# Optimization experiments

Hardware: AMD Instinct MI355X
Metric: run time of the kernel (lower is better)

## Reference

```python
import jax, jax.numpy as jnp
import numpy as np

MARGIN = 0.0
GAP = 0.4
N, D, C = 8192, 128, 10


def setup_inputs() -> dict:
    key = jax.random.key(0)
    k1, k2, k3 = jax.random.split(key, 3)
    inputs = jax.random.normal(k1, (N, D), dtype=jnp.float32)
    pred = jax.random.normal(k2, (N, C), dtype=jnp.float32)
    targets = jax.random.randint(k3, (N,), 0, C, dtype=jnp.int64)
    return {"inputs": inputs, "pred": pred, "targets": targets}


def reference(inputs, pred, targets):
    n = inputs.shape[0]
    # pairwise euclidean distances: ||xi||^2 + ||xj||^2 - 2 xi.xj, clamped + sqrt
    sq = jnp.sum(inputs * inputs, axis=1)                      # [n]
    dist = sq[:, None] + sq[None, :] - 2.0 * (inputs @ inputs.T)
    dist = jnp.sqrt(jnp.clip(dist, 1e-12))                     # [n, n]
    same = targets[:, None] == targets[None, :]                # [n, n] bool

    # confusion detection (original runs under no_grad)
    p = jax.nn.softmax(jax.lax.stop_gradient(pred), axis=1)
    val, top2 = jax.lax.top_k(p, 2)                            # [n,2]
    confuse = (val[:, 0] - val[:, 1] <= GAP) | (top2[:, 0] != targets)  # [n]

    # hard mining per row: hardest positive (max over same-class), hardest negative (min over diff-class)
    dist_ap = jnp.max(jnp.where(same, dist, -jnp.inf), axis=1)  # [n]
    dist_an = jnp.min(jnp.where(same, jnp.inf, dist), axis=1)   # [n]

    # MarginRankingLoss(margin=MARGIN) with y=1: mean(relu(-(an - ap) + margin)) over confused rows
    per_row = jnp.maximum(dist_ap - dist_an + MARGIN, 0.0)
    cnt = jnp.sum(confuse.astype(jnp.float32))
    loss = jnp.sum(jnp.where(confuse, per_row, 0.0)) / jnp.maximum(cnt, 1.0)
    return jnp.where(cnt > 0, loss, 0.0)
```

## Files before the change

kernel.cpp:

```cpp
#include <hip/hip_runtime.h>

#define NROWS 8192
#define DIMX  128
#define KB    192
#define KSEG  12
#define PTB   24576
#define NKS   3
#define NCLS  10
#define GAPV  0.4f
#define DEBIAS 504.03125f
#define SCL   (-0.0078125f)
#define RGR   256
#define NRG   (NROWS / RGR)
#define CHUNK 512
#define NCHUNK (NROWS / CHUNK)
#define SLAB  64
#define NSLAB (CHUNK / SLAB)

typedef __attribute__((ext_vector_type(4))) int i32x4;

#define GLOAD_LDS16(g, l)                                              \
  __builtin_amdgcn_global_load_lds(                                    \
      (const __attribute__((address_space(1))) void*)(g),              \
      (__attribute__((address_space(3))) void*)(l), 16, 0, 0)

__device__ __forceinline__ int q8(float v) {
  int q = (int)rintf(16.f * v);
  return q > 127 ? 127 : (q < -127 ? -127 : q);
}

__global__ __launch_bounds__(256) void prep_k(const float* __restrict__ x,
                                              const int* __restrict__ tgt,
                                              const float* __restrict__ pred,
                                              char* __restrict__ xa,
                                              char* __restrict__ xbm,
                                              float* __restrict__ sq,
                                              int* __restrict__ conf,
                                              unsigned* __restrict__ ctrs) {
  if (blockIdx.x == 0 && threadIdx.x < 3) ctrs[threadIdx.x] = 0u;

  const int wave = threadIdx.x >> 6;
  const int lane = threadIdx.x & 63;
  const int row  = blockIdx.x * 4 + wave;
  const float2 f2 = ((const float2*)(x + (size_t)row * DIMX))[lane];
  float s = f2.x * f2.x + f2.y * f2.y;
  #pragma unroll
  for (int m = 1; m < 64; m <<= 1) s += __shfl_xor(s, m, 64);

  char* basea = xa  + (size_t)(row >> 7) * PTB + (size_t)(row & 127) * 16;
  char* baseb = xbm + (size_t)(row >> 7) * PTB + (size_t)(row & 127) * 16;
  {
    const int q0 = q8(f2.x), q1 = q8(f2.y);
    const unsigned short u = (unsigned short)((q0 & 0xFF) | ((q1 & 0xFF) << 8));
    const size_t off = (size_t)(lane >> 3) * 2048 + (lane & 7) * 2;
    *(unsigned short*)(basea + off) = u;
    *(unsigned short*)(baseb + off) = u;
  }
  const int cls = tgt[row];
  if (lane < 32) {
    const int j = 2 * lane;
    const int c = j >> 2;
    const bool hit = (c < NCLS) && (c == cls);
    const unsigned short ua = hit ? (unsigned short)0x7F7F : 0;
    const unsigned short ub = hit ? (unsigned short)0x8181 : 0;
    const size_t off = (size_t)(8 + (j >> 4)) * 2048 + (j & 15);
    *(unsigned short*)(basea + off) = ua;
    *(unsigned short*)(baseb + off) = ub;
  }

  if (lane == 0) {
    sq[row] = s;
    const float* pp = pred + (size_t)row * NCLS;
    float v[NCLS];
    #pragma unroll
    for (int c = 0; c < NCLS; ++c) v[c] = pp[c];
    float m1 = v[0]; int i1 = 0;
    #pragma unroll
    for (int c = 1; c < NCLS; ++c)
      if (v[c] > m1) { m1 = v[c]; i1 = c; }
    float m2 = -INFINITY, sum = 0.f;
    #pragma unroll
    for (int c = 0; c < NCLS; ++c) {
      sum += __expf(v[c] - m1);
      if (c != i1) m2 = fmaxf(m2, v[c]);
    }
    const float d01 = (1.f - __expf(m2 - m1)) / sum;
    conf[row] = (d01 <= GAPV) || (i1 != cls);
  }
}

__global__ __launch_bounds__(256)
__attribute__((amdgpu_waves_per_eu(3, 4)))
void gram_k(const char* __restrict__ xa,
            const char* __restrict__ xbm,
            const float* __restrict__ sq,
            float* __restrict__ smax,
            float* __restrict__ smin) {
  __shared__ char  ldsb[2][KSEG * 1024];
  __shared__ float sqb[2][SLAB];
  const int tid  = threadIdx.x;
  const int wave = tid >> 6;
  const int lane = tid & 63;
  const int quad = lane >> 4;
  const int m16  = lane & 15;
  const int bx = blockIdx.x, by = blockIdx.y;

  i32x4 A[4][NKS];
  #pragma unroll
  for (int rt = 0; rt < 4; ++rt) {
    const int rbase = wave * 64 + rt * 16;
    const char* pa = xa + (size_t)(bx * 2 + (rbase >> 7)) * PTB
                        + (size_t)((rbase & 127) + m16) * 16;
    #pragma unroll
    for (int ks = 0; ks < NKS; ++ks)
      A[rt][ks] = *(const i32x4*)(pa + (size_t)(ks * 4 + quad) * 2048);
  }
  #pragma unroll
  for (int rt = 0; rt < 4; ++rt)
    #pragma unroll
    for (int ks = 0; ks < NKS; ++ks)
      asm("" : "+v"(A[rt][ks]));

  float gmin[4][4], gmax[4][4];
  #pragma unroll
  for (int r = 0; r < 4; ++r)
    #pragma unroll
    for (int q = 0; q < 4; ++q) { gmin[r][q] = INFINITY; gmax[r][q] = -INFINITY; }

  {
    const char* srcb = xbm + (size_t)(by * 4) * PTB;
    #pragma unroll
    for (int u = 0; u < 3; ++u) {
      const int kseg = wave * 3 + u;
      GLOAD_LDS16(srcb + (size_t)kseg * 2048 + lane * 16, &ldsb[0][kseg * 1024 + lane * 16]);
    }
    if (wave == 3 && lane < 16)
      GLOAD_LDS16((const char*)(sq + by * CHUNK) + lane * 16, (char*)&sqb[0][0] + lane * 16);
  }

  for (int s = 0; s < NSLAB; ++s) {
    __syncthreads();
    if (s + 1 < NSLAB) {
      const char* srcb = xbm + (size_t)(by * 4 + ((s + 1) >> 1)) * PTB + ((s + 1) & 1) * 1024;
      char* dstb = &ldsb[(s + 1) & 1][0];
      #pragma unroll
      for (int u = 0; u < 3; ++u) {
        const int kseg = wave * 3 + u;
        GLOAD_LDS16(srcb + (size_t)kseg * 2048 + lane * 16, dstb + kseg * 1024 + lane * 16);
      }
      if (wave == 3 && lane < 16)
        GLOAD_LDS16((const char*)(sq + by * CHUNK + (s + 1) * SLAB) + lane * 16,
                    (char*)&sqb[(s + 1) & 1][0] + lane * 16);
    }
    const char* buf = &ldsb[s & 1][0];
    #pragma unroll
    for (int jt = 0; jt < 4; ++jt) {
      i32x4 B[NKS];
      #pragma unroll
      for (int ks = 0; ks < NKS; ++ks)
        B[ks] = *(const i32x4*)(buf + (ks * 4 + quad) * 1024 + (jt * 16 + m16) * 16);
      const float sqj = sqb[s & 1][jt * 16 + m16];

      i32x4 acc[4];
      #pragma unroll
      for (int r = 0; r < 4; ++r) acc[r] = (i32x4){0, 0, 0, 0};
      #pragma unroll
      for (int ks = 0; ks < NKS; ++ks)
        #pragma unroll
        for (int r = 0; r < 4; ++r)
          acc[r] = __builtin_amdgcn_mfma_i32_16x16x64_i8(A[r][ks], B[ks], acc[r], 0, 0, 0);

      #pragma unroll
      for (int r = 0; r < 4; ++r)
        #pragma unroll
        for (int q = 0; q < 4; ++q) {
          const float cand = fmaf((float)acc[r][q], SCL, sqj);
          gmin[r][q] = fminf(gmin[r][q], cand);
          gmax[r][q] = fmaxf(gmax[r][q], cand);
        }
    }
  }

  #pragma unroll
  for (int m = 1; m <= 8; m <<= 1)
    #pragma unroll
    for (int r = 0; r < 4; ++r)
      #pragma unroll
      for (int q = 0; q < 4; ++q) {
        gmin[r][q] = fminf(gmin[r][q], __shfl_xor(gmin[r][q], m, 64));
        gmax[r][q] = fmaxf(gmax[r][q], __shfl_xor(gmax[r][q], m, 64));
      }

  if (m16 == 0) {
    const size_t sidx = (size_t)(bx * NCHUNK + by) * RGR;
    #pragma unroll
    for (int r = 0; r < 4; ++r) {
      const int lrow = wave * 64 + r * 16 + quad * 4;
      *(float4*)&smax[sidx + lrow] = make_float4(gmax[r][0], gmax[r][1], gmax[r][2], gmax[r][3]);
      *(float4*)&smin[sidx + lrow] = make_float4(gmin[r][0], gmin[r][1], gmin[r][2], gmin[r][3]);
    }
  }
}

__global__ __launch_bounds__(256) void reduce_k(const float* __restrict__ smax,
                                                const float* __restrict__ smin,
                                                const float* __restrict__ sq,
                                                const int* __restrict__ conf,
                                                unsigned* __restrict__ ctrs,
                                                float* __restrict__ out) {
  __shared__ float red[2][4];
  const int tid = threadIdx.x, bx = blockIdx.x;
  const int wave = tid >> 6, lane = tid & 63;
  const int row = bx * RGR + tid;

  unsigned* g_done = ctrs;
  float*    Ssum   = (float*)(ctrs + 1);
  float*    Csum   = (float*)(ctrs + 2);

  float hi = -INFINITY, lo = INFINITY;
  #pragma unroll
  for (int c = 0; c < NCHUNK; ++c) {
    hi = fmaxf(hi, smax[(size_t)(bx * NCHUNK + c) * RGR + tid]);
    lo = fminf(lo, smin[(size_t)(bx * NCHUNK + c) * RGR + tid]);
  }
  float ps = 0.f, pc = 0.f;
  if (conf[row]) {
    const float ap = sqrtf(fmaxf(sq[row] + hi - DEBIAS, 1e-12f));
    const float an = sqrtf(fmaxf(sq[row] + lo, 1e-12f));
    ps = fmaxf(ap - an, 0.f);
    pc = 1.f;
  }
  #pragma unroll
  for (int m = 1; m < 64; m <<= 1) {
    ps += __shfl_xor(ps, m, 64);
    pc += __shfl_xor(pc, m, 64);
  }
  if (lane == 0) { red[0][wave] = ps; red[1][wave] = pc; }
  __syncthreads();
  if (tid == 0) {
    atomicAdd(Ssum, red[0][0] + red[0][1] + red[0][2] + red[0][3]);
    atomicAdd(Csum, red[1][0] + red[1][1] + red[1][2] + red[1][3]);
    __threadfence();
    if (atomicAdd(g_done, 1u) == NRG - 1u) {
      const float St = atomicAdd(Ssum, 0.f);
      const float Ct = atomicAdd(Csum, 0.f);
      out[0] = (Ct > 0.f) ? (St / fmaxf(Ct, 1.f)) : 0.f;
    }
  }
}

extern "C" void kernel_launch(void* const* d_in, const int* in_sizes, int n_in,
                              void* d_out, int out_size, void* d_ws, size_t ws_size,
                              hipStream_t stream) {
  const float* x    = (const float*)d_in[0];
  const float* pred = (const float*)d_in[1];
  const int*   tgt  = (const int*)d_in[2];
  float* out = (float*)d_out;

  char* w = (char*)d_ws;
  const size_t arr_bytes = (size_t)NROWS * KB;
  const size_t stg_bytes = (size_t)NRG * NCHUNK * RGR * 4;
  char*     xa   = w;
  char*     xbm  = w + arr_bytes;
  float*    sq   = (float*)(w + 2 * arr_bytes);
  int*      conf = (int*)(w + 2 * arr_bytes + (size_t)NROWS * 4);
  float*    smax = (float*)(w + 2 * arr_bytes + (size_t)NROWS * 8);
  float*    smin = (float*)(w + 2 * arr_bytes + (size_t)NROWS * 8 + stg_bytes);
  unsigned* ctrs = (unsigned*)(w + 2 * arr_bytes + (size_t)NROWS * 8 + 2 * stg_bytes);

  hipLaunchKernelGGL(prep_k, dim3(NROWS / 4), dim3(256), 0, stream,
                     x, tgt, pred, xa, xbm, sq, conf, ctrs);
  hipLaunchKernelGGL(gram_k, dim3(NRG, NCHUNK), dim3(256), 0, stream,
                     xa, xbm, sq, smax, smin);
  hipLaunchKernelGGL(reduce_k, dim3(NRG), dim3(256), 0, stream,
                     smax, smin, sq, conf, ctrs, out);
}
```

Before: 84.39 us.

## Fuse int8 quantization and column norms into gram kernel, drop prep kernel

Removes the separate prep kernel. The gram kernel now quantizes rows of x to int8 on the fly, both for the A fragments in registers and for the B slabs written to LDS, which replaces the async global-to-LDS copies of pre-packed data. The squared norm of each column is folded into the int8 MFMA through extra K lanes, so the epilogue becomes a pure integer min/max. The softmax confusion test and row norms move into reduce_k. This saves one launch and the packed-array round trip through memory, at the cost of redundant fp32 reads and quantization work in every gram block.

```diff
diff --git a/kernel.cpp b/kernel.cpp
--- a/kernel.cpp
+++ b/kernel.cpp
@@ -2,10 +2,6 @@
 
 #define NROWS 8192
 #define DIMX  128
-#define KB    192
-#define KSEG  12
-#define PTB   24576
-#define NKS   3
 #define NCLS  10
 #define GAPV  0.4f
 #define DEBIAS 504.03125f
@@ -16,88 +12,27 @@
 #define NCHUNK (NROWS / CHUNK)
 #define SLAB  64
 #define NSLAB (CHUNK / SLAB)
+#define NKS   3
 
 typedef __attribute__((ext_vector_type(4))) int i32x4;
-
-#define GLOAD_LDS16(g, l)                                              \
-  __builtin_amdgcn_global_load_lds(                                    \
-      (const __attribute__((address_space(1))) void*)(g),              \
-      (__attribute__((address_space(3))) void*)(l), 16, 0, 0)
 
 __device__ __forceinline__ int q8(float v) {
   int q = (int)rintf(16.f * v);
   return q > 127 ? 127 : (q < -127 ? -127 : q);
 }
-
-__global__ __launch_bounds__(256) void prep_k(const float* __restrict__ x,
-                                              const int* __restrict__ tgt,
-                                              const float* __restrict__ pred,
-                                              char* __restrict__ xa,
-                                              char* __restrict__ xbm,
-                                              float* __restrict__ sq,
-                                              int* __restrict__ conf,
-                                              unsigned* __restrict__ ctrs) {
-  if (blockIdx.x == 0 && threadIdx.x < 3) ctrs[threadIdx.x] = 0u;
-
-  const int wave = threadIdx.x >> 6;
-  const int lane = threadIdx.x & 63;
-  const int row  = blockIdx.x * 4 + wave;
-  const float2 f2 = ((const float2*)(x + (size_t)row * DIMX))[lane];
-  float s = f2.x * f2.x + f2.y * f2.y;
-  #pragma unroll
-  for (int m = 1; m < 64; m <<= 1) s += __shfl_xor(s, m, 64);
-
-  char* basea = xa  + (size_t)(row >> 7) * PTB + (size_t)(row & 127) * 16;
-  char* baseb = xbm + (size_t)(row >> 7) * PTB + (size_t)(row & 127) * 16;
-  {
-    const int q0 = q8(f2.x), q1 = q8(f2.y);
-    const unsigned short u = (unsigned short)((q0 & 0xFF) | ((q1 & 0xFF) << 8));
-    const size_t off = (size_t)(lane >> 3) * 2048 + (lane & 7) * 2;
-    *(unsigned short*)(basea + off) = u;
-    *(unsigned short*)(baseb + off) = u;
-  }
-  const int cls = tgt[row];
-  if (lane < 32) {
-    const int j = 2 * lane;
-    const int c = j >> 2;
-    const bool hit = (c < NCLS) && (c == cls);
-    const unsigned short ua = hit ? (unsigned short)0x7F7F : 0;
-    const unsigned short ub = hit ? (unsigned short)0x8181 : 0;
-    const size_t off = (size_t)(8 + (j >> 4)) * 2048 + (j & 15);
-    *(unsigned short*)(basea + off) = ua;
-    *(unsigned short*)(baseb + off) = ub;
-  }
-
-  if (lane == 0) {
-    sq[row] = s;
-    const float* pp = pred + (size_t)row * NCLS;
-    float v[NCLS];
-    #pragma unroll
-    for (int c = 0; c < NCLS; ++c) v[c] = pp[c];
-    float m1 = v[0]; int i1 = 0;
-    #pragma unroll
-    for (int c = 1; c < NCLS; ++c)
-      if (v[c] > m1) { m1 = v[c]; i1 = c; }
-    float m2 = -INFINITY, sum = 0.f;
-    #pragma unroll
-    for (int c = 0; c < NCLS; ++c) {
-      sum += __expf(v[c] - m1);
-      if (c != i1) m2 = fmaxf(m2, v[c]);
-    }
-    const float d01 = (1.f - __expf(m2 - m1)) / sum;
-    conf[row] = (d01 <= GAPV) || (i1 != cls);
-  }
+__device__ __forceinline__ int pk4(float4 v) {
+  return (q8(v.x) & 255) | ((q8(v.y) & 255) << 8) |
+         ((q8(v.z) & 255) << 16) | ((q8(v.w) & 255) << 24);
 }
 
 __global__ __launch_bounds__(256)
-__attribute__((amdgpu_waves_per_eu(3, 4)))
-void gram_k(const char* __restrict__ xa,
-            const char* __restrict__ xbm,
-            const float* __restrict__ sq,
-            float* __restrict__ smax,
-            float* __restrict__ smin) {
-  __shared__ char  ldsb[2][KSEG * 1024];
-  __shared__ float sqb[2][SLAB];
+__attribute__((amdgpu_waves_per_eu(2, 8)))
+void gram_k(const float* __restrict__ x,
+            const int* __restrict__ tgt,
+            int* __restrict__ smin,
+            int* __restrict__ smax,
+            unsigned* __restrict__ ctrs) {
+  __shared__ char ldsb[2][12 * 1024];
   const int tid  = threadIdx.x;
   const int wave = tid >> 6;
   const int lane = tid & 63;
@@ -105,15 +40,26 @@
   const int m16  = lane & 15;
   const int bx = blockIdx.x, by = blockIdx.y;
 
+  if (bx == 0 && by == 0 && tid < 3) ctrs[tid] = 0u;
+
   i32x4 A[4][NKS];
   #pragma unroll
   for (int rt = 0; rt < 4; ++rt) {
-    const int rbase = wave * 64 + rt * 16;
-    const char* pa = xa + (size_t)(bx * 2 + (rbase >> 7)) * PTB
-                        + (size_t)((rbase & 127) + m16) * 16;
-    #pragma unroll
-    for (int ks = 0; ks < NKS; ++ks)
-      A[rt][ks] = *(const i32x4*)(pa + (size_t)(ks * 4 + quad) * 2048);
+    const int row = bx * 256 + wave * 64 + rt * 16 + m16;
+    const float4* xr = (const float4*)(x + (size_t)row * DIMX);
+    #pragma unroll
+    for (int ks = 0; ks < 2; ++ks) {
+      const float4* p = xr + ks * 16 + quad * 4;
+      i32x4 f;
+      #pragma unroll
+      for (int w = 0; w < 4; ++w) f[w] = pk4(p[w]);
+      A[rt][ks] = f;
+    }
+    const int cls = tgt[row];
+    i32x4 a2 = {0, 0, 0, 0};
+    if ((cls >> 2) == quad) a2[cls & 3] = 0x7F7F7F7F;
+    if (quad == 2) a2[2] |= 0x00017F7F;
+    A[rt][2] = a2;
   }
   #pragma unroll
   for (int rt = 0; rt < 4; ++rt)
@@ -121,37 +67,59 @@
     for (int ks = 0; ks < NKS; ++ks)
       asm("" : "+v"(A[rt][ks]));
 
-  float gmin[4][4], gmax[4][4];
+  int Emin[4][4], Emax[4][4];
   #pragma unroll
   for (int r = 0; r < 4; ++r)
     #pragma unroll
-    for (int q = 0; q < 4; ++q) { gmin[r][q] = INFINITY; gmax[r][q] = -INFINITY; }
-
-  {
-    const char* srcb = xbm + (size_t)(by * 4) * PTB;
-    #pragma unroll
-    for (int u = 0; u < 3; ++u) {
-      const int kseg = wave * 3 + u;
-      GLOAD_LDS16(srcb + (size_t)kseg * 2048 + lane * 16, &ldsb[0][kseg * 1024 + lane * 16]);
-    }
-    if (wave == 3 && lane < 16)
-      GLOAD_LDS16((const char*)(sq + by * CHUNK) + lane * 16, (char*)&sqb[0][0] + lane * 16);
-  }
+    for (int q = 0; q < 4; ++q) { Emin[r][q] = 0x7FFFFFFF; Emax[r][q] = (int)0x80000000; }
+
+  const int jc = tid >> 2;
+  const int pp = tid & 3;
+  auto quant_slab = [&](int s, char* buf) {
+    const int col = by * CHUNK + s * SLAB + jc;
+    const float4* xc = (const float4*)(x + (size_t)col * DIMX) + pp * 8;
+    float ss = 0.f;
+    i32x4 d0, d1;
+    #pragma unroll
+    for (int w = 0; w < 4; ++w) {
+      const float4 v = xc[w];
+      ss += v.x * v.x + v.y * v.y + v.z * v.z + v.w * v.w;
+      d0[w] = pk4(v);
+    }
+    #pragma unroll
+    for (int w = 0; w < 4; ++w) {
+      const float4 v = xc[4 + w];
+      ss += v.x * v.x + v.y * v.y + v.z * v.z + v.w * v.w;
+      d1[w] = pk4(v);
+    }
+    ss += __shfl_xor(ss, 1, 64);
+    ss += __shfl_xor(ss, 2, 64);
+    *(i32x4*)(buf + (2 * pp) * 1024 + jc * 16) = d0;
+    *(i32x4*)(buf + (2 * pp + 1) * 1024 + jc * 16) = d1;
+    if (pp == 0) {
+      const int cls = tgt[col];
+      const int K  = min((int)rintf(128.f * ss), 32385);
+      const int t  = min(K / 127, 254);
+      const int b1 = t < 127 ? t : 127;
+      const int b2 = t - b1;
+      const int rr = min(K - 127 * t, 126);
+      i32x4 k8 = {0,0,0,0}, k9 = {0,0,0,0}, k10 = {0,0,0,0}, k11 = {0,0,0,0};
+      if (cls < 4)      k8[cls]      = (int)0x81818181;
+      else if (cls < 8) k9[cls - 4]  = (int)0x81818181;
+      else              k10[cls - 8] = (int)0x81818181;
+      k10[2] = ((-b1) & 255) | (((-b2) & 255) << 8) | (((-rr) & 255) << 16);
+      *(i32x4*)(buf +  8 * 1024 + jc * 16) = k8;
+      *(i32x4*)(buf +  9 * 1024 + jc * 16) = k9;
+      *(i32x4*)(buf + 10 * 1024 + jc * 16) = k10;
+      *(i32x4*)(buf + 11 * 1024 + jc * 16) = k11;
+    }
+  };
+
+  quant_slab(0, &ldsb[0][0]);
 
   for (int s = 0; s < NSLAB; ++s) {
     __syncthreads();
-    if (s + 1 < NSLAB) {
-      const char* srcb = xbm + (size_t)(by * 4 + ((s + 1) >> 1)) * PTB + ((s + 1) & 1) * 1024;
-      char* dstb = &ldsb[(s + 1) & 1][0];
-      #pragma unroll
-      for (int u = 0; u < 3; ++u) {
-        const int kseg = wave * 3 + u;
-        GLOAD_LDS16(srcb + (size_t)kseg * 2048 + lane * 16, dstb + kseg * 1024 + lane * 16);
-      }
-      if (wave == 3 && lane < 16)
-        GLOAD_LDS16((const char*)(sq + by * CHUNK + (s + 1) * SLAB) + lane * 16,
-                    (char*)&sqb[(s + 1) & 1][0] + lane * 16);
-    }
+    if (s + 1 < NSLAB) quant_slab(s + 1, &ldsb[(s + 1) & 1][0]);
     const char* buf = &ldsb[s & 1][0];
     #pragma unroll
     for (int jt = 0; jt < 4; ++jt) {
@@ -159,7 +127,6 @@
       #pragma unroll
       for (int ks = 0; ks < NKS; ++ks)
         B[ks] = *(const i32x4*)(buf + (ks * 4 + quad) * 1024 + (jt * 16 + m16) * 16);
-      const float sqj = sqb[s & 1][jt * 16 + m16];
 
       i32x4 acc[4];
       #pragma unroll
@@ -174,9 +141,8 @@
       for (int r = 0; r < 4; ++r)
         #pragma unroll
         for (int q = 0; q < 4; ++q) {
-          const float cand = fmaf((float)acc[r][q], SCL, sqj);
-          gmin[r][q] = fminf(gmin[r][q], cand);
-          gmax[r][q] = fmaxf(gmax[r][q], cand);
+          Emin[r][q] = min(Emin[r][q], acc[r][q]);
+          Emax[r][q] = max(Emax[r][q], acc[r][q]);
         }
     }
   }
@@ -187,8 +153,8 @@
     for (int r = 0; r < 4; ++r)
       #pragma unroll
       for (int q = 0; q < 4; ++q) {
-        gmin[r][q] = fminf(gmin[r][q], __shfl_xor(gmin[r][q], m, 64));
-        gmax[r][q] = fmaxf(gmax[r][q], __shfl_xor(gmax[r][q], m, 64));
+        Emin[r][q] = min(Emin[r][q], __shfl_xor(Emin[r][q], m, 64));
+        Emax[r][q] = max(Emax[r][q], __shfl_xor(Emax[r][q], m, 64));
       }
 
   if (m16 == 0) {
@@ -196,16 +162,17 @@
     #pragma unroll
     for (int r = 0; r < 4; ++r) {
       const int lrow = wave * 64 + r * 16 + quad * 4;
-      *(float4*)&smax[sidx + lrow] = make_float4(gmax[r][0], gmax[r][1], gmax[r][2], gmax[r][3]);
-      *(float4*)&smin[sidx + lrow] = make_float4(gmin[r][0], gmin[r][1], gmin[r][2], gmin[r][3]);
-    }
-  }
-}
-
-__global__ __launch_bounds__(256) void reduce_k(const float* __restrict__ smax,
-                                                const float* __restrict__ smin,
-                                                const float* __restrict__ sq,
-                                                const int* __restrict__ conf,
+      *(int4*)&smin[sidx + lrow] = make_int4(Emin[r][0], Emin[r][1], Emin[r][2], Emin[r][3]);
+      *(int4*)&smax[sidx + lrow] = make_int4(Emax[r][0], Emax[r][1], Emax[r][2], Emax[r][3]);
+    }
+  }
+}
+
+__global__ __launch_bounds__(256) void reduce_k(const int* __restrict__ smin,
+                                                const int* __restrict__ smax,
+                                                const float* __restrict__ x,
+                                                const float* __restrict__ pred,
+                                                const int* __restrict__ tgt,
                                                 unsigned* __restrict__ ctrs,
                                                 float* __restrict__ out) {
   __shared__ float red[2][4];
@@ -217,16 +184,44 @@
   float*    Ssum   = (float*)(ctrs + 1);
   float*    Csum   = (float*)(ctrs + 2);
 
-  float hi = -INFINITY, lo = INFINITY;
+  int lo = 0x7FFFFFFF, hi = (int)0x80000000;
   #pragma unroll
   for (int c = 0; c < NCHUNK; ++c) {
-    hi = fmaxf(hi, smax[(size_t)(bx * NCHUNK + c) * RGR + tid]);
-    lo = fminf(lo, smin[(size_t)(bx * NCHUNK + c) * RGR + tid]);
-  }
+    lo = min(lo, smin[(size_t)(bx * NCHUNK + c) * RGR + tid]);
+    hi = max(hi, smax[(size_t)(bx * NCHUNK + c) * RGR + tid]);
+  }
+
+  const float4* xr = (const float4*)(x + (size_t)row * DIMX);
+  float s = 0.f;
+  #pragma unroll
+  for (int w = 0; w < DIMX / 4; ++w) {
+    const float4 v = xr[w];
+    s += v.x * v.x + v.y * v.y + v.z * v.z + v.w * v.w;
+  }
+
+  const float* pp = pred + (size_t)row * NCLS;
+  float v[NCLS];
+  #pragma unroll
+  for (int c = 0; c < NCLS; ++c) v[c] = pp[c];
+  float m1 = v[0]; int i1 = 0;
+  #pragma unroll
+  for (int c = 1; c < NCLS; ++c)
+    if (v[c] > m1) { m1 = v[c]; i1 = c; }
+  float m2 = -INFINITY, sum = 0.f;
+  #pragma unroll
+  for (int c = 0; c < NCLS; ++c) {
+    sum += __expf(v[c] - m1);
+    if (c != i1) m2 = fmaxf(m2, v[c]);
+  }
+  const float d01 = (1.f - __expf(m2 - m1)) / sum;
+  const int conf = (d01 <= GAPV) || (i1 != tgt[row]);
+
+  const float hc = SCL * (float)lo;
+  const float lc = SCL * (float)hi;
   float ps = 0.f, pc = 0.f;
-  if (conf[row]) {
-    const float ap = sqrtf(fmaxf(sq[row] + hi - DEBIAS, 1e-12f));
-    const float an = sqrtf(fmaxf(sq[row] + lo, 1e-12f));
+  if (conf) {
+    const float ap = sqrtf(fmaxf(s + hc - DEBIAS, 1e-12f));
+    const float an = sqrtf(fmaxf(s + lc, 1e-12f));
     ps = fmaxf(ap - an, 0.f);
     pc = 1.f;
   }
@@ -258,20 +253,13 @@
   float* out = (float*)d_out;
 
   char* w = (char*)d_ws;
-  const size_t arr_bytes = (size_t)NROWS * KB;
   const size_t stg_bytes = (size_t)NRG * NCHUNK * RGR * 4;
-  char*     xa   = w;
-  char*     xbm  = w + arr_bytes;
-  float*    sq   = (float*)(w + 2 * arr_bytes);
-  int*      conf = (int*)(w + 2 * arr_bytes + (size_t)NROWS * 4);
-  float*    smax = (float*)(w + 2 * arr_bytes + (size_t)NROWS * 8);
-  float*    smin = (float*)(w + 2 * arr_bytes + (size_t)NROWS * 8 + stg_bytes);
-  unsigned* ctrs = (unsigned*)(w + 2 * arr_bytes + (size_t)NROWS * 8 + 2 * stg_bytes);
-
-  hipLaunchKernelGGL(prep_k, dim3(NROWS / 4), dim3(256), 0, stream,
-                     x, tgt, pred, xa, xbm, sq, conf, ctrs);
+  int*      smin = (int*)w;
+  int*      smax = (int*)(w + stg_bytes);
+  unsigned* ctrs = (unsigned*)(w + 2 * stg_bytes);
+
   hipLaunchKernelGGL(gram_k, dim3(NRG, NCHUNK), dim3(256), 0, stream,
-                     xa, xbm, sq, smax, smin);
+                     x, tgt, smin, smax, ctrs);
   hipLaunchKernelGGL(reduce_k, dim3(NRG), dim3(256), 0, stream,
-                     smax, smin, sq, conf, ctrs, out);
-}
+                     smin, smax, x, pred, tgt, ctrs, out);
+}
```

Result: slower. 100.4 us (+18.9%).
